# Performance work log

Hardware: AMD Instinct MI355X
Metric: run time of the kernel (lower is better)

## Reference

```python
import jax, jax.numpy as jnp
import numpy as np
from jax import lax

EPS = 1e-5

def conv2d(x, w, b=None, pad=1):
    # x: [N,C,H,W], w: [O,I,kh,kw]
    out = lax.conv_general_dilated(x, w, window_strides=(1, 1),
                                   padding=[(pad, pad), (pad, pad)],
                                   dimension_numbers=('NCHW', 'OIHW', 'NCHW'))
    if b is not None:
        out = out + b[None, :, None, None]
    return out

def batchnorm(x, gamma, beta):
    # training-mode BN (biased batch stats), matching torch default train()
    mean = jnp.mean(x, axis=(0, 2, 3), keepdims=True)
    var = jnp.var(x, axis=(0, 2, 3), keepdims=True)
    xn = (x - mean) * lax.rsqrt(var + EPS)
    return xn * gamma[None, :, None, None] + beta[None, :, None, None]

def setup_inputs() -> dict:
    key = jax.random.key(0)
    ks = jax.random.split(key, 16)
    B, Cin, H, W = 4, 3, 256, 256
    Cout = 128
    NP = 32
    npat = NP // 3  # 10 per normal region
    qc_in = Cout + 3 * npat + NP  # 190 (actual concat width)

    def kaiming(k, shape, fan_in):
        return jax.random.normal(k, shape, jnp.float32) * np.sqrt(2.0 / fan_in)

    inp = {
        'x': jax.random.normal(ks[0], (B, Cin, H, W), jnp.float32),
        'conv1_w': kaiming(ks[1], (Cout // 2, Cin, 3, 3), Cin * 9),
        'conv1_b': jnp.zeros((Cout // 2,), jnp.float32),
        'bn1_g': jnp.ones((Cout // 2,), jnp.float32),
        'bn1_b': jnp.zeros((Cout // 2,), jnp.float32),
        'conv2_w': kaiming(ks[2], (Cout, Cout // 2, 3, 3), (Cout // 2) * 9),
        'conv2_b': jnp.zeros((Cout,), jnp.float32),
        'bn2_g': jnp.ones((Cout,), jnp.float32),
        'bn2_b': jnp.zeros((Cout,), jnp.float32),
        'core_p': jax.random.normal(ks[3], (npat, Cout, 3, 3), jnp.float32),
        'clad_p': jax.random.normal(ks[4], (npat, Cout, 3, 3), jnp.float32),
        'ferr_p': jax.random.normal(ks[5], (npat, Cout, 3, 3), jnp.float32),
        'anom_p': jax.random.normal(ks[6], (NP, Cout, 3, 3), jnp.float32),
        'qa1_w': kaiming(ks[7], (64, qc_in, 1, 1), qc_in),
        'qa1_b': jnp.zeros((64,), jnp.float32),
        'qa2_w': kaiming(ks[8], (1, 64, 1, 1), 64),
        'qa2_b': jnp.zeros((1,), jnp.float32),
        'cls_w': kaiming(ks[9], (4, qc_in, 1, 1), qc_in),
        'cls_b': jnp.zeros((4,), jnp.float32),
    }
    return inp

def reference(x, conv1_w, conv1_b, bn1_g, bn1_b, conv2_w, conv2_b, bn2_g, bn2_b,
              core_p, clad_p, ferr_p, anom_p, qa1_w, qa1_b, qa2_w, qa2_b, cls_w, cls_b):
    # feature extractor: conv-bn-relu x2
    h = jax.nn.relu(batchnorm(conv2d(x, conv1_w, conv1_b), bn1_g, bn1_b))
    features = jax.nn.relu(batchnorm(conv2d(h, conv2_w, conv2_b), bn2_g, bn2_b))

    # pattern matching: the per-pattern loop of 1-out-channel convs + sigmoid
    # is exactly one multi-output-channel conv (no bias) + sigmoid
    normal_w = jnp.concatenate([core_p, clad_p, ferr_p], axis=0)  # [30,C,3,3]
    all_matches = jax.nn.sigmoid(conv2d(features, normal_w))       # [B,30,H,W]
    anomaly_matches = jax.nn.sigmoid(conv2d(features, anom_p))     # [B,32,H,W]

    quality_input = jnp.concatenate([features, all_matches, anomaly_matches], axis=1)
    q = jax.nn.relu(conv2d(quality_input, qa1_w, qa1_b, pad=0))
    quality_scores = jax.nn.sigmoid(conv2d(q, qa2_w, qa2_b, pad=0))

    classifications = conv2d(quality_input, cls_w, cls_b, pad=0)
    region_logits = classifications[:, :3]
    anomaly_logits = classifications[:, 3:4]
    region_probs = jax.nn.softmax(region_logits, axis=1)
    anomaly_probs = jax.nn.sigmoid(anomaly_logits)

    return (features, region_logits, anomaly_logits, all_matches,
            anomaly_matches, quality_scores, region_probs, anomaly_probs)
```

## Files before the change

### kernel.cpp

```cpp
#include <hip/hip_runtime.h>
#include <hip/hip_bf16.h>

typedef unsigned short u16;
typedef __attribute__((ext_vector_type(8)))  short s8v;
typedef __attribute__((ext_vector_type(4)))  short s4v;
typedef __attribute__((ext_vector_type(16))) float f16v;

#define HWX 65536
#define EPSV 1e-5f

#define O0 0u
#define O1 33554432u
#define O2 34340864u
#define O3 34603008u
#define O4 42467328u
#define O5 50855936u
#define O6 51118080u
#define O7 51904512u

__device__ __forceinline__ float u2f(u16 u) {
    union { unsigned int i; float f; } v; v.i = ((unsigned int)u) << 16; return v.f;
}
__device__ __forceinline__ u16 f2u(float f) {
    __hip_bfloat16 h = __float2bfloat16(f);
    return *reinterpret_cast<u16*>(&h);
}
__device__ __forceinline__ s8v ld8(const u16* p) {
    union { s8v v; s4v h[2]; } r;
    r.h[0] = *(const s4v*)p;
    r.h[1] = *(const s4v*)(p + 4);
    return r.v;
}

#define PHYS(i) ((i) + ((i) >> 5))

__global__ __launch_bounds__(256) void k_conv1(const float* __restrict__ x,
                                               const float* __restrict__ w,
                                               const float* __restrict__ bias,
                                               u16* __restrict__ out,
                                               float* __restrict__ ssum,
                                               float* __restrict__ sqsum) {
    const int h = blockIdx.x, cb = blockIdx.y, b = blockIdx.z;
    const int t = threadIdx.x;
    const int pg = t & 31, cg = t >> 5;
    const int px0 = pg * 8, c0 = cg * 4;
    const int cbase = cb * 32;

    __shared__ float xs[3][3][266];
    __shared__ float wl[27 * 33];

    float acc[4][8];
    #pragma unroll
    for (int c = 0; c < 4; c++) {
        float bv = bias[cbase + c0 + c];
        #pragma unroll
        for (int p = 0; p < 8; p++) acc[c][p] = bv;
    }

    for (int idx = t; idx < 3 * 768; idx += 256) {
        int ci = idx / 768, rem = idx - ci * 768;
        int r = rem >> 8, px = rem & 255;
        int hh = h + r - 1;
        float v = 0.f;
        if ((unsigned)hh < 256u)
            v = x[((size_t)(b * 3 + ci) * 256 + hh) * 256 + px];
        xs[ci][r][PHYS(1 + px)] = v;
    }
    if (t < 18) {
        int ci = t / 6, rr = t - ci * 6;
        xs[ci][rr >> 1][(rr & 1) ? PHYS(257) : 0] = 0.f;
    }
    for (int idx = t; idx < 27 * 32; idx += 256) {
        int co = idx / 27, rem = idx - co * 27;
        wl[rem * 33 + co] = w[(cbase + co) * 27 + rem];
    }
    __syncthreads();

    for (int ci = 0; ci < 3; ci++) {
        #pragma unroll
        for (int kh = 0; kh < 3; kh++) {
            float xv[10];
            #pragma unroll
            for (int j = 0; j < 10; j++) xv[j] = xs[ci][kh][PHYS(px0 + j)];
            float wv[3][4];
            #pragma unroll
            for (int kw = 0; kw < 3; kw++)
                #pragma unroll
                for (int c = 0; c < 4; c++)
                    wv[kw][c] = wl[(ci * 9 + kh * 3 + kw) * 33 + c0 + c];
            #pragma unroll
            for (int c = 0; c < 4; c++)
                #pragma unroll
                for (int p = 0; p < 8; p++)
                    acc[c][p] += xv[p] * wv[0][c] + xv[p + 1] * wv[1][c]
                               + xv[p + 2] * wv[2][c];
        }
    }

    #pragma unroll
    for (int c = 0; c < 4; c++) {
        int cm = cbase + c0 + c;
        u16* op = out + (((size_t)(b * 64 + cm) * 256 + h) * 256 + px0);
        #pragma unroll
        for (int p = 0; p < 8; p++) op[p] = f2u(acc[c][p]);
    }

    __syncthreads();
    float* red = &xs[0][0][0];
    #pragma unroll
    for (int c = 0; c < 4; c++) {
        float sv = 0.f, qv = 0.f;
        #pragma unroll
        for (int p = 0; p < 8; p++) { sv += acc[c][p]; qv += acc[c][p] * acc[c][p]; }
        red[(c0 + c) * 33 + pg] = sv;
        red[1056 + (c0 + c) * 33 + pg] = qv;
    }
    __syncthreads();
    if (t < 64) {
        int co = t & 31, v = t >> 5;
        const float* base = red + v * 1056 + co * 33;
        float sum = 0.f;
        #pragma unroll
        for (int i = 0; i < 32; i++) sum += base[i];
        atomicAdd((v ? sqsum : ssum) + cbase + co, sum);
    }
}

__global__ void k_finalize(const float* __restrict__ s, const float* __restrict__ q,
                           const float* __restrict__ g, const float* __restrict__ be,
                           float* __restrict__ sc, float* __restrict__ sh, int C) {
    int c = threadIdx.x;
    if (c >= C) return;
    const float invN = 1.f / 262144.f;
    float m = s[c] * invN;
    float v = fmaxf(q[c] * invN - m * m, 0.f);
    float scale = g[c] * rsqrtf(v + EPSV);
    sc[c] = scale;
    sh[c] = be[c] - m * scale;
}

__global__ __launch_bounds__(256) void k_bnrelu_h(ushort4* __restrict__ buf,
                                                  const float* __restrict__ sc,
                                                  const float* __restrict__ sh) {
    size_t i = (size_t)blockIdx.x * 256 + threadIdx.x;
    int c = (int)(i >> 14) & 63;
    float s = sc[c], h0 = sh[c];
    ushort4 r = buf[i];
    ushort4 o;
    o.x = f2u(fmaxf(u2f(r.x) * s + h0, 0.f));
    o.y = f2u(fmaxf(u2f(r.y) * s + h0, 0.f));
    o.z = f2u(fmaxf(u2f(r.z) * s + h0, 0.f));
    o.w = f2u(fmaxf(u2f(r.w) * s + h0, 0.f));
    buf[i] = o;
}

__global__ __launch_bounds__(256) void k_bnrelu(float4* __restrict__ buf,
                                                const float* __restrict__ sc,
                                                const float* __restrict__ sh, int C) {
    size_t i = (size_t)blockIdx.x * 256 + threadIdx.x;
    int c = (int)(i >> 14) % C;
    float s = sc[c], h0 = sh[c];
    float4 r = buf[i];
    float4 o;
    o.x = fmaxf(r.x * s + h0, 0.f);
    o.y = fmaxf(r.y * s + h0, 0.f);
    o.z = fmaxf(r.z * s + h0, 0.f);
    o.w = fmaxf(r.w * s + h0, 0.f);
    buf[i] = o;
}

__global__ __launch_bounds__(256) void k_stats(const float* __restrict__ raw,
                                               float* __restrict__ ssum,
                                               float* __restrict__ sqsum) {
    const int co = blockIdx.x, seg = blockIdx.y;
    const int t = threadIdx.x;
    __shared__ float red[8];
    float s = 0.f, q = 0.f;
    for (int b = 0; b < 4; b++) {
        const float4* p = (const float4*)(raw + ((size_t)(b * 128 + co) * HWX) + seg * 8192);
        for (int i = t; i < 2048; i += 256) {
            float4 v = p[i];
            s += v.x + v.y + v.z + v.w;
            q += v.x * v.x + v.y * v.y + v.z * v.z + v.w * v.w;
        }
    }
    #pragma unroll
    for (int off = 32; off; off >>= 1) {
        s += __shfl_down(s, off, 64);
        q += __shfl_down(q, off, 64);
    }
    int lane = t & 63, wv = t >> 6;
    if (lane == 0) { red[wv] = s; red[4 + wv] = q; }
    __syncthreads();
    if (t == 0) atomicAdd(&ssum[co], red[0] + red[1] + red[2] + red[3]);
    else if (t == 1) atomicAdd(&sqsum[co], red[4] + red[5] + red[6] + red[7]);
}

__global__ void k_prep_w(const float* __restrict__ wcat, u16* __restrict__ wtile) {
    int i = blockIdx.x * 256 + threadIdx.x;
    if (i >= 159744) return;
    int ch = i / 19968, rem = i - ch * 19968;
    int pl = rem / 9984; rem -= pl * 9984;
    int kwco = rem / 52, k = rem - kwco * 52;
    int kw = kwco >> 6, co = kwco & 63;
    u16 v = 0;
    if (k < 48 && co < 62) {
        int kh = k >> 4, ci = ch * 16 + (k & 15);
        float f = wcat[(size_t)co * 1152 + ci * 9 + kh * 3 + kw];
        u16 hv = f2u(f);
        v = pl ? f2u(f - u2f(hv)) : hv;
    }
    wtile[i] = v;
}
__global__ void k_prep_w2(const float* __restrict__ w2, u16* __restrict__ wtile2) {
    int i = blockIdx.x * 256 + threadIdx.x;
    if (i >= 79872) return;
    int ch = i / 19968, rem = i - ch * 19968;
    int kwco = rem / 52, k = rem - kwco * 52;
    int kw = kwco >> 7, co = kwco & 127;
    u16 v = 0;
    if (k < 48) {
        int kh = k >> 4, ci = ch * 16 + (k & 15);
        v = f2u(w2[((size_t)co * 64 + ci) * 9 + kh * 3 + kw]);
    }
    wtile2[i] = v;
}
__global__ void k_prep_wh(const float* __restrict__ qa1w, const float* __restrict__ clsw,
                          u16* __restrict__ whl) {
    int i = blockIdx.x * 256 + threadIdx.x;
    if (i >= 46080) return;
    int ch = i / 3840, rem = i - ch * 3840;
    int pl = rem / 1920; rem -= pl * 1920;
    int co = rem / 20, kloc = rem - co * 20;
    u16 v = 0;
    int k = ch * 16 + kloc;
    if (kloc < 16 && k < 190 && co < 68) {
        float f = (co < 64) ? qa1w[co * 190 + k] : clsw[(co - 64) * 190 + k];
        u16 hv = f2u(f);
        v = pl ? f2u(f - u2f(hv)) : hv;
    }
    whl[i] = v;
}

__device__ __forceinline__ void load_x_c2(const u16* __restrict__ hb, int b, int ch,
                                          int h, int t, unsigned xp[24]) {
    #pragma unroll
    for (int r = 0; r < 3; r++) {
        int hh = h + r - 1;
        bool vr = (unsigned)hh < 256u;
        if (vr) {
            const u16* base = hb + ((size_t)(b * 64 + ch * 16) << 16)
                            + ((size_t)hh << 8) + t;
            #pragma unroll
            for (int ci = 0; ci < 16; ci += 2) {
                unsigned a = base[(size_t)ci << 16];
                unsigned c = base[(size_t)(ci + 1) << 16];
                xp[(r * 16 + ci) >> 1] = a | (c << 16);
            }
        } else {
            #pragma unroll
            for (int ci = 0; ci < 16; ci += 2) xp[(r * 16 + ci) >> 1] = 0u;
        }
    }
}

__device__ __forceinline__ void load_split_match(const float* __restrict__ feat,
                                                 int b, int ch, int h0, int t,
                                                 unsigned xhi[32], unsigned xlo[32]) {
    #pragma unroll
    for (int r = 0; r < 4; r++) {
        int hh = h0 + r - 1;
        if ((unsigned)hh < 256u) {
            const float* base = feat + ((size_t)(b * 128 + ch * 16) << 16)
                              + ((size_t)hh << 8) + t;
            float v[16];
            #pragma unroll
            for (int ci = 0; ci < 16; ci++)
                v[ci] = base[(size_t)ci << 16];
            #pragma unroll
            for (int ci = 0; ci < 16; ci += 2) {
                u16 ha = f2u(v[ci]), hb2 = f2u(v[ci + 1]);
                unsigned la = f2u(v[ci] - u2f(ha));
                unsigned lb = f2u(v[ci + 1] - u2f(hb2));
                xhi[(r * 16 + ci) >> 1] = (unsigned)ha | ((unsigned)hb2 << 16);
                xlo[(r * 16 + ci) >> 1] = la | (lb << 16);
            }
        }
    }
}

__global__ __launch_bounds__(256, 2) void k_conv2_mf(
    const u16* __restrict__ hb, const u16* __restrict__ wtile2,
    const float* __restrict__ bias, float* __restrict__ out)
{
    const int h = blockIdx.x, b = blockIdx.y;
    const int t = threadIdx.x, l = t & 63, wv = t >> 6;
    const int kg = (l >> 5) * 8, nn = l & 31;

    __shared__ __align__(16) u16 xs[258 * 52];
    __shared__ __align__(16) u16 wl[3 * 128 * 52];

    f16v acc[2][4];
    #pragma unroll
    for (int pt = 0; pt < 2; pt++)
        #pragma unroll
        for (int s = 0; s < 4; s++)
            #pragma unroll
            for (int r = 0; r < 16; r++) acc[pt][s][r] = 0.f;

    for (int i = t; i < 258 * 52 / 4; i += 256)
        ((ushort4*)xs)[i] = ushort4{0, 0, 0, 0};
    __syncthreads();

    unsigned xp[24];
    load_x_c2(hb, b, 0, h, t, xp);

    for (int ch = 0; ch < 4; ch++) {
        {
            const int4* src = (const int4*)(wtile2 + (size_t)ch * 19968);
            for (int i = t; i < 2496; i += 256) ((int4*)wl)[i] = src[i];
        }
        #pragma unroll
        for (int r = 0; r < 3; r++) {
            if ((unsigned)(h + r - 1) < 256u) {
                #pragma unroll
                for (int g = 0; g < 4; g++) {
                    int i0 = r * 16 + g * 4;
                    uint2 hp;
                    hp.x = xp[i0 >> 1];
                    hp.y = xp[(i0 >> 1) + 1];
                    *(uint2*)&xs[(size_t)(t + 1) * 52 + i0] = hp;
                }
            }
        }
        __syncthreads();
        if (ch < 3) load_x_c2(hb, b, ch + 1, h, t, xp);
        #pragma unroll
        for (int kw = 0; kw < 3; kw++) {
            #pragma unroll
            for (int ks = 0; ks < 3; ks++) {
                int k0 = ks * 16 + kg;
                s8v af[4], bf[2];
                #pragma unroll
                for (int s = 0; s < 4; s++)
                    af[s] = ld8(&wl[(kw * 128 + s * 32 + nn) * 52 + k0]);
                #pragma unroll
                for (int pt = 0; pt < 2; pt++)
                    bf[pt] = ld8(&xs[((wv * 2 + pt) * 32 + nn + kw) * 52 + k0]);
                #pragma unroll
                for (int pt = 0; pt < 2; pt++)
                    #pragma unroll
                    for (int s = 0; s < 4; s++)
                        acc[pt][s] = __builtin_amdgcn_mfma_f32_32x32x16_bf16(
                            af[s], bf[pt], acc[pt][s], 0, 0, 0);
            }
        }
        __syncthreads();
    }

    #pragma unroll
    for (int pt = 0; pt < 2; pt++) {
        int px = (wv * 2 + pt) * 32 + nn;
        #pragma unroll
        for (int s = 0; s < 4; s++) {
            #pragma unroll
            for (int r = 0; r < 16; r++) {
                int co = s * 32 + (r & 3) + 8 * (r >> 2) + 4 * (l >> 5);
                out[(((size_t)b * 128 + co) * 256 + h) * 256 + px] = acc[pt][s][r] + bias[co];
            }
        }
    }
}

__global__ __launch_bounds__(256, 2) void k_match_mf(
    const float* __restrict__ feat, const u16* __restrict__ wtile,
    float* __restrict__ out_all, float* __restrict__ out_anom)
{
    const int h0 = blockIdx.x * 2, b = blockIdx.y;
    const int t = threadIdx.x, l = t & 63, wv = t >> 6;
    const int kg = (l >> 5) * 8, nn = l & 31;

    __shared__ __align__(16) u16 xr[4 * 258 * 20];
    __shared__ __align__(16) u16 wl[2 * 9984];

    f16v acc[2][2][2];
    #pragma unroll
    for (int o = 0; o < 2; o++)
        #pragma unroll
        for (int pt = 0; pt < 2; pt++)
            #pragma unroll
            for (int s = 0; s < 2; s++)
                #pragma unroll
                for (int r = 0; r < 16; r++) acc[o][pt][s][r] = 0.f;

    for (int i = t; i < 4 * 258 * 20 / 4; i += 256)
        ((ushort4*)xr)[i] = ushort4{0, 0, 0, 0};
    __syncthreads();

    unsigned xhi[32], xlo[32];
    load_split_match(feat, b, 0, h0, t, xhi, xlo);

    for (int ch = 0; ch < 8; ch++) {
        {
            const int4* src = (const int4*)(wtile + (size_t)ch * 2 * 9984);
            for (int i = t; i < 2496; i += 256) ((int4*)wl)[i] = src[i];
        }
        #pragma unroll
        for (int r = 0; r < 4; r++) {
            if ((unsigned)(h0 + r - 1) < 256u) {
                u16* dst = xr + r * 5160 + (t + 1) * 20;
                #pragma unroll
                for (int g = 0; g < 4; g++) {
                    uint2 hp;
                    hp.x = xhi[r * 8 + g * 2];
                    hp.y = xhi[r * 8 + g * 2 + 1];
                    *(uint2*)&dst[g * 4] = hp;
                }
            }
        }
        __syncthreads();
        #pragma unroll
        for (int kw = 0; kw < 3; kw++) {
            #pragma unroll
            for (int ks = 0; ks < 3; ks++) {
                int k0 = ks * 16 + kg;
                s8v ah0 = ld8(&wl[(kw * 64 + nn) * 52 + k0]);
                s8v ah1 = ld8(&wl[(kw * 64 + 32 + nn) * 52 + k0]);
                s8v al0 = ld8(&wl[9984 + (kw * 64 + nn) * 52 + k0]);
                s8v al1 = ld8(&wl[9984 + (kw * 64 + 32 + nn) * 52 + k0]);
                #pragma unroll
                for (int o = 0; o < 2; o++) {
                    #pragma unroll
                    for (int pt = 0; pt < 2; pt++) {
                        s8v xf = ld8(&xr[(ks + o) * 5160
                                         + ((wv * 2 + pt) * 32 + nn + kw) * 20 + kg]);
                        acc[o][pt][0] = __builtin_amdgcn_mfma_f32_32x32x16_bf16(ah0, xf, acc[o][pt][0], 0, 0, 0);
                        acc[o][pt][0] = __builtin_amdgcn_mfma_f32_32x32x16_bf16(al0, xf, acc[o][pt][0], 0, 0, 0);
                        acc[o][pt][1] = __builtin_amdgcn_mfma_f32_32x32x16_bf16(ah1, xf, acc[o][pt][1], 0, 0, 0);
                        acc[o][pt][1] = __builtin_amdgcn_mfma_f32_32x32x16_bf16(al1, xf, acc[o][pt][1], 0, 0, 0);
                    }
                }
            }
        }
        __syncthreads();
        #pragma unroll
        for (int r = 0; r < 4; r++) {
            if ((unsigned)(h0 + r - 1) < 256u) {
                u16* dst = xr + r * 5160 + (t + 1) * 20;
                #pragma unroll
                for (int g = 0; g < 4; g++) {
                    uint2 lp;
                    lp.x = xlo[r * 8 + g * 2];
                    lp.y = xlo[r * 8 + g * 2 + 1];
                    *(uint2*)&dst[g * 4] = lp;
                }
            }
        }
        __syncthreads();
        if (ch < 7) load_split_match(feat, b, ch + 1, h0, t, xhi, xlo);
        #pragma unroll
        for (int kw = 0; kw < 3; kw++) {
            #pragma unroll
            for (int ks = 0; ks < 3; ks++) {
                int k0 = ks * 16 + kg;
                s8v ah0 = ld8(&wl[(kw * 64 + nn) * 52 + k0]);
                s8v ah1 = ld8(&wl[(kw * 64 + 32 + nn) * 52 + k0]);
                #pragma unroll
                for (int o = 0; o < 2; o++) {
                    #pragma unroll
                    for (int pt = 0; pt < 2; pt++) {
                        s8v xf = ld8(&xr[(ks + o) * 5160
                                         + ((wv * 2 + pt) * 32 + nn + kw) * 20 + kg]);
                        acc[o][pt][0] = __builtin_amdgcn_mfma_f32_32x32x16_bf16(ah0, xf, acc[o][pt][0], 0, 0, 0);
                        acc[o][pt][1] = __builtin_amdgcn_mfma_f32_32x32x16_bf16(ah1, xf, acc[o][pt][1], 0, 0, 0);
                    }
                }
            }
        }
        __syncthreads();
    }

    #pragma unroll
    for (int o = 0; o < 2; o++) {
        int h = h0 + o;
        #pragma unroll
        for (int pt = 0; pt < 2; pt++) {
            int px = (wv * 2 + pt) * 32 + nn;
            #pragma unroll
            for (int s = 0; s < 2; s++) {
                #pragma unroll
                for (int r = 0; r < 16; r++) {
                    int cm = s * 32 + (r & 3) + 8 * (r >> 2) + 4 * (l >> 5);
                    float sg = 1.f / (1.f + __expf(-acc[o][pt][s][r]));
                    if (cm < 30)
                        out_all[(((size_t)b * 30 + cm) * 256 + h) * 256 + px] = sg;
                    else if (cm < 62)
                        out_anom[(((size_t)b * 32 + cm - 30) * 256 + h) * 256 + px] = sg;
                }
            }
        }
    }
}

__device__ __forceinline__ void load_x_heads(const float* __restrict__ fb,
                                             const float* __restrict__ ab,
                                             const float* __restrict__ nb,
                                             int ch, float xv[16]) {
    #pragma unroll
    for (int ci = 0; ci < 16; ci++) {
        int k = ch * 16 + ci;
        float v;
        if (k < 128)      v = fb[(size_t)k << 16];
        else if (k < 158) v = ab[(size_t)(k - 128) << 16];
        else if (k < 190) v = nb[(size_t)(k - 158) << 16];
        else              v = 0.f;
        xv[ci] = v;
    }
}

__global__ __launch_bounds__(256, 2) void k_heads_mf(
    const float* __restrict__ dout, const u16* __restrict__ whl,
    const float* __restrict__ qa1b, const float* __restrict__ qa2w,
    const float* __restrict__ qa2b, const float* __restrict__ clsb,
    float* __restrict__ out)
{
    const int h = blockIdx.x, b = blockIdx.y;
    const int t = threadIdx.x, l = t & 63, wv = t >> 6;
    const int kg = (l >> 5) * 8, nn = l & 31;

    __shared__ __align__(16) u16 xh[256 * 20];
    __shared__ __align__(16) u16 xl[256 * 20];
    __shared__ __align__(16) u16 wl2[2 * 1920];
    __shared__ float lb[69];
    __shared__ float lw2[64];

    if (t < 64) { lb[t] = qa1b[t]; lw2[t] = qa2w[t]; }
    if (t < 4) lb[64 + t] = clsb[t];
    if (t == 0) lb[68] = qa2b[0];

    f16v acc[3][2];
    #pragma unroll
    for (int s = 0; s < 3; s++)
        #pragma unroll
        for (int pt = 0; pt < 2; pt++)
            #pragma unroll
            for (int r = 0; r < 16; r++) acc[s][pt][r] = 0.f;

    const float* fb = dout + O0 + (((size_t)b * 128) << 16) + ((size_t)h << 8) + t;
    const float* ab = dout + O3 + (((size_t)b * 30) << 16) + ((size_t)h << 8) + t;
    const float* nb = dout + O4 + (((size_t)b * 32) << 16) + ((size_t)h << 8) + t;

    float xv[16];
    load_x_heads(fb, ab, nb, 0, xv);

    #pragma unroll
    for (int ch = 0; ch < 12; ch++) {
        {
            const int4* src = (const int4*)(whl + (size_t)ch * 3840);
            for (int i = t; i < 480; i += 256) ((int4*)wl2)[i] = src[i];
        }
        #pragma unroll
        for (int g = 0; g < 4; g++) {
            int i0 = g * 4;
            u16 h0 = f2u(xv[i0 + 0]), h1 = f2u(xv[i0 + 1]);
            u16 h2 = f2u(xv[i0 + 2]), h3 = f2u(xv[i0 + 3]);
            uint2 hp, lp;
            hp.x = (unsigned)h0 | ((unsigned)h1 << 16);
            hp.y = (unsigned)h2 | ((unsigned)h3 << 16);
            lp.x = (unsigned)f2u(xv[i0 + 0] - u2f(h0))
                 | ((unsigned)f2u(xv[i0 + 1] - u2f(h1)) << 16);
            lp.y = (unsigned)f2u(xv[i0 + 2] - u2f(h2))
                 | ((unsigned)f2u(xv[i0 + 3] - u2f(h3)) << 16);
            *(uint2*)&xh[t * 20 + i0] = hp;
            *(uint2*)&xl[t * 20 + i0] = lp;
        }
        __syncthreads();
        if (ch < 11) load_x_heads(fb, ab, nb, ch + 1, xv);
        s8v xfh[2], xfl[2];
        #pragma unroll
        for (int pt = 0; pt < 2; pt++) {
            int row = (wv * 2 + pt) * 32 + nn;
            xfh[pt] = ld8(&xh[row * 20 + kg]);
            xfl[pt] = ld8(&xl[row * 20 + kg]);
        }
        #pragma unroll
        for (int s = 0; s < 3; s++) {
            s8v awh = ld8(&wl2[(s * 32 + nn) * 20 + kg]);
            s8v awl = ld8(&wl2[1920 + (s * 32 + nn) * 20 + kg]);
            #pragma unroll
            for (int pt = 0; pt < 2; pt++) {
                acc[s][pt] = __builtin_amdgcn_mfma_f32_32x32x16_bf16(awh, xfh[pt], acc[s][pt], 0, 0, 0);
                acc[s][pt] = __builtin_amdgcn_mfma_f32_32x32x16_bf16(awl, xfh[pt], acc[s][pt], 0, 0, 0);
                acc[s][pt] = __builtin_amdgcn_mfma_f32_32x32x16_bf16(awh, xfl[pt], acc[s][pt], 0, 0, 0);
            }
        }
        __syncthreads();
    }

    const int hi = l >> 5;
    #pragma unroll
    for (int pt = 0; pt < 2; pt++) {
        float qa_part = 0.f;
        #pragma unroll
        for (int m = 0; m < 2; m++)
            #pragma unroll
            for (int r = 0; r < 16; r++) {
                int row = m * 32 + (r & 3) + 8 * (r >> 2) + 4 * hi;
                float v = acc[m][pt][r] + lb[row];
                qa_part += fmaxf(v, 0.f) * lw2[row];
            }
        qa_part += __shfl_xor(qa_part, 32, 64);
        if (hi == 0) {
            int px = (wv * 2 + pt) * 32 + nn;
            size_t hw = (size_t)h * 256 + px;
            float quality = 1.f / (1.f + __expf(-(qa_part + lb[68])));
            float c0 = acc[2][pt][0] + lb[64];
            float c1 = acc[2][pt][1] + lb[65];
            float c2 = acc[2][pt][2] + lb[66];
            float c3 = acc[2][pt][3] + lb[67];
            float m0 = fmaxf(c0, fmaxf(c1, c2));
            float e0 = __expf(c0 - m0), e1 = __expf(c1 - m0), e2 = __expf(c2 - m0);
            float inv = 1.f / (e0 + e1 + e2);
            out[O1 + ((size_t)b * 3 + 0) * HWX + hw] = c0;
            out[O1 + ((size_t)b * 3 + 1) * HWX + hw] = c1;
            out[O1 + ((size_t)b * 3 + 2) * HWX + hw] = c2;
            out[O2 + (size_t)b * HWX + hw] = c3;
            out[O5 + (size_t)b * HWX + hw] = quality;
            out[O6 + ((size_t)b * 3 + 0) * HWX + hw] = e0 * inv;
            out[O6 + ((size_t)b * 3 + 1) * HWX + hw] = e1 * inv;
            out[O6 + ((size_t)b * 3 + 2) * HWX + hw] = e2 * inv;
            out[O7 + (size_t)b * HWX + hw] = 1.f / (1.f + __expf(-c3));
        }
    }
}

extern "C" void kernel_launch(void* const* d_in, const int* in_sizes, int n_in,
                              void* d_out, int out_size, void* d_ws, size_t ws_size,
                              hipStream_t stream) {
    (void)in_sizes; (void)n_in; (void)out_size; (void)ws_size;
    const float* x    = (const float*)d_in[0];
    const float* w1   = (const float*)d_in[1];
    const float* b1   = (const float*)d_in[2];
    const float* g1   = (const float*)d_in[3];
    const float* be1  = (const float*)d_in[4];
    const float* w2   = (const float*)d_in[5];
    const float* b2   = (const float*)d_in[6];
    const float* g2   = (const float*)d_in[7];
    const float* be2  = (const float*)d_in[8];
    const float* core = (const float*)d_in[9];
    const float* clad = (const float*)d_in[10];
    const float* ferr = (const float*)d_in[11];
    const float* anom = (const float*)d_in[12];
    const float* qa1w = (const float*)d_in[13];
    const float* qa1b = (const float*)d_in[14];
    const float* qa2w = (const float*)d_in[15];
    const float* qa2b = (const float*)d_in[16];
    const float* clsw = (const float*)d_in[17];
    const float* clsb = (const float*)d_in[18];

    char* ws = (char*)d_ws;
    float* stats = (float*)ws;
    float* s1 = stats + 0;
    float* q1 = stats + 64;
    float* s2 = stats + 128;
    float* q2 = stats + 256;
    float* sc1 = stats + 384;
    float* sh1 = stats + 448;
    float* sc2 = stats + 512;
    float* sh2 = stats + 640;
    u16*   hraw   = (u16*)(ws + 4096);
    float* wcat   = (float*)(ws + 33558528ull);
    u16*   wtile2 = (u16*)(ws + 33844224ull);
    u16*   wtile  = (u16*)(ws + 34004224ull);
    u16*   whl    = (u16*)wcat;
    float* dout = (float*)d_out;

    hipMemsetAsync(stats, 0, 384 * sizeof(float), stream);
    hipMemcpyAsync(wcat,             core, 10 * 1152 * 4, hipMemcpyDeviceToDevice, stream);
    hipMemcpyAsync(wcat + 10 * 1152, clad, 10 * 1152 * 4, hipMemcpyDeviceToDevice, stream);
    hipMemcpyAsync(wcat + 20 * 1152, ferr, 10 * 1152 * 4, hipMemcpyDeviceToDevice, stream);
    hipMemcpyAsync(wcat + 30 * 1152, anom, 32 * 1152 * 4, hipMemcpyDeviceToDevice, stream);

    dim3 blk(256);
    k_prep_w2<<<312, blk, 0, stream>>>(w2, wtile2);
    k_prep_w<<<624, blk, 0, stream>>>(wcat, wtile);
    k_prep_wh<<<180, blk, 0, stream>>>(qa1w, clsw, whl);

    k_conv1<<<dim3(256, 2, 4), blk, 0, stream>>>(x, w1, b1, hraw, s1, q1);
    k_finalize<<<1, 128, 0, stream>>>(s1, q1, g1, be1, sc1, sh1, 64);
    k_bnrelu_h<<<16384, blk, 0, stream>>>((ushort4*)hraw, sc1, sh1);

    k_conv2_mf<<<dim3(256, 4), blk, 0, stream>>>(hraw, wtile2, b2, dout + O0);
    k_stats<<<dim3(128, 8), blk, 0, stream>>>(dout + O0, s2, q2);
    k_finalize<<<1, 128, 0, stream>>>(s2, q2, g2, be2, sc2, sh2, 128);
    k_bnrelu<<<32768, blk, 0, stream>>>((float4*)(dout + O0), sc2, sh2, 128);

    k_match_mf<<<dim3(128, 4), blk, 0, stream>>>(dout + O0, wtile, dout + O3, dout + O4);
    k_heads_mf<<<dim3(256, 4), blk, 0, stream>>>(dout, whl, qa1b, qa2w, qa2b, clsb, dout);
}
```

Measured before the change: 610.2 us.

## Fuse BN2 statistics into conv2 epilogue and finalize into bnrelu

Conv2 now reduces per-channel sum and sum of squares in its epilogue with wave shuffles, an LDS reduction and atomics. This removes the separate stats kernel, which re-read the whole 128MB feature map. The BN finalize step is folded into the bnrelu kernel, which recomputes scale and shift per thread. The heads kernel's launch bounds are also raised to target 3 blocks per SM. The conv2 epilogue takes on extra shuffle work and more atomic traffic, and the tighter register limit on the heads kernel risks spills.

```diff
diff --git a/kernel.cpp b/kernel.cpp
--- a/kernel.cpp
+++ b/kernel.cpp
@@ -155,45 +155,24 @@
 }
 
 __global__ __launch_bounds__(256) void k_bnrelu(float4* __restrict__ buf,
-                                                const float* __restrict__ sc,
-                                                const float* __restrict__ sh, int C) {
+                                                const float* __restrict__ s,
+                                                const float* __restrict__ q,
+                                                const float* __restrict__ g,
+                                                const float* __restrict__ be, int C) {
     size_t i = (size_t)blockIdx.x * 256 + threadIdx.x;
     int c = (int)(i >> 14) % C;
-    float s = sc[c], h0 = sh[c];
+    const float invN = 1.f / 262144.f;
+    float m = s[c] * invN;
+    float var = fmaxf(q[c] * invN - m * m, 0.f);
+    float sc = g[c] * rsqrtf(var + EPSV);
+    float sh = be[c] - m * sc;
     float4 r = buf[i];
     float4 o;
-    o.x = fmaxf(r.x * s + h0, 0.f);
-    o.y = fmaxf(r.y * s + h0, 0.f);
-    o.z = fmaxf(r.z * s + h0, 0.f);
-    o.w = fmaxf(r.w * s + h0, 0.f);
+    o.x = fmaxf(r.x * sc + sh, 0.f);
+    o.y = fmaxf(r.y * sc + sh, 0.f);
+    o.z = fmaxf(r.z * sc + sh, 0.f);
+    o.w = fmaxf(r.w * sc + sh, 0.f);
     buf[i] = o;
-}
-
-__global__ __launch_bounds__(256) void k_stats(const float* __restrict__ raw,
-                                               float* __restrict__ ssum,
-                                               float* __restrict__ sqsum) {
-    const int co = blockIdx.x, seg = blockIdx.y;
-    const int t = threadIdx.x;
-    __shared__ float red[8];
-    float s = 0.f, q = 0.f;
-    for (int b = 0; b < 4; b++) {
-        const float4* p = (const float4*)(raw + ((size_t)(b * 128 + co) * HWX) + seg * 8192);
-        for (int i = t; i < 2048; i += 256) {
-            float4 v = p[i];
-            s += v.x + v.y + v.z + v.w;
-            q += v.x * v.x + v.y * v.y + v.z * v.z + v.w * v.w;
-        }
-    }
-    #pragma unroll
-    for (int off = 32; off; off >>= 1) {
-        s += __shfl_down(s, off, 64);
-        q += __shfl_down(q, off, 64);
-    }
-    int lane = t & 63, wv = t >> 6;
-    if (lane == 0) { red[wv] = s; red[4 + wv] = q; }
-    __syncthreads();
-    if (t == 0) atomicAdd(&ssum[co], red[0] + red[1] + red[2] + red[3]);
-    else if (t == 1) atomicAdd(&sqsum[co], red[4] + red[5] + red[6] + red[7]);
 }
 
 __global__ void k_prep_w(const float* __restrict__ wcat, u16* __restrict__ wtile) {
@@ -291,7 +270,8 @@
 
 __global__ __launch_bounds__(256, 2) void k_conv2_mf(
     const u16* __restrict__ hb, const u16* __restrict__ wtile2,
-    const float* __restrict__ bias, float* __restrict__ out)
+    const float* __restrict__ bias, float* __restrict__ out,
+    float* __restrict__ ssum, float* __restrict__ sqsum)
 {
     const int h = blockIdx.x, b = blockIdx.y;
     const int t = threadIdx.x, l = t & 63, wv = t >> 6;
@@ -358,17 +338,49 @@
         __syncthreads();
     }
 
-    #pragma unroll
-    for (int pt = 0; pt < 2; pt++) {
-        int px = (wv * 2 + pt) * 32 + nn;
-        #pragma unroll
-        for (int s = 0; s < 4; s++) {
-            #pragma unroll
-            for (int r = 0; r < 16; r++) {
-                int co = s * 32 + (r & 3) + 8 * (r >> 2) + 4 * (l >> 5);
-                out[(((size_t)b * 128 + co) * 256 + h) * 256 + px] = acc[pt][s][r] + bias[co];
-            }
-        }
+    float* red = (float*)xs;
+    const int hi = l >> 5;
+    const int px0 = (wv * 2 + 0) * 32 + nn;
+    const int px1 = (wv * 2 + 1) * 32 + nn;
+    #pragma unroll
+    for (int s = 0; s < 4; s++) {
+        #pragma unroll
+        for (int r = 0; r < 16; r++) {
+            int co = s * 32 + (r & 3) + 8 * (r >> 2) + 4 * hi;
+            float bv = bias[co];
+            float v0 = acc[0][s][r] + bv;
+            float v1 = acc[1][s][r] + bv;
+            size_t base = (((size_t)b * 128 + co) * 256 + h) * 256;
+            out[base + px0] = v0;
+            out[base + px1] = v1;
+            float ps = v0 + v1, pq = v0 * v0 + v1 * v1;
+            #pragma unroll
+            for (int off = 16; off; off >>= 1) {
+                ps += __shfl_xor(ps, off, 64);
+                pq += __shfl_xor(pq, off, 64);
+            }
+            if (nn == 0) {
+                int slot = (wv * 2 + hi) * 64 + s * 16 + r;
+                red[slot] = ps;
+                red[512 + slot] = pq;
+            }
+        }
+    }
+    __syncthreads();
+    if (t < 128) {
+        int co = t;
+        int w32 = co & 31, si = co >> 5;
+        int hib = (w32 >> 2) & 1;
+        int ri = (w32 & 3) | (((w32 >> 3) & 3) << 2);
+        float as = 0.f, aq = 0.f;
+        #pragma unroll
+        for (int w = 0; w < 4; w++) {
+            int slot = (w * 2 + hib) * 64 + si * 16 + ri;
+            as += red[slot];
+            aq += red[512 + slot];
+        }
+        atomicAdd(&ssum[co], as);
+        atomicAdd(&sqsum[co], aq);
     }
 }
 
@@ -518,7 +530,7 @@
     }
 }
 
-__global__ __launch_bounds__(256, 2) void k_heads_mf(
+__global__ __launch_bounds__(256, 3) void k_heads_mf(
     const float* __restrict__ dout, const u16* __restrict__ whl,
     const float* __restrict__ qa1b, const float* __restrict__ qa2w,
     const float* __restrict__ qa2b, const float* __restrict__ clsb,
@@ -666,8 +678,6 @@
     float* q2 = stats + 256;
     float* sc1 = stats + 384;
     float* sh1 = stats + 448;
-    float* sc2 = stats + 512;
-    float* sh2 = stats + 640;
     u16*   hraw   = (u16*)(ws + 4096);
     float* wcat   = (float*)(ws + 33558528ull);
     u16*   wtile2 = (u16*)(ws + 33844224ull);
@@ -690,10 +700,8 @@
     k_finalize<<<1, 128, 0, stream>>>(s1, q1, g1, be1, sc1, sh1, 64);
     k_bnrelu_h<<<16384, blk, 0, stream>>>((ushort4*)hraw, sc1, sh1);
 
-    k_conv2_mf<<<dim3(256, 4), blk, 0, stream>>>(hraw, wtile2, b2, dout + O0);
-    k_stats<<<dim3(128, 8), blk, 0, stream>>>(dout + O0, s2, q2);
-    k_finalize<<<1, 128, 0, stream>>>(s2, q2, g2, be2, sc2, sh2, 128);
-    k_bnrelu<<<32768, blk, 0, stream>>>((float4*)(dout + O0), sc2, sh2, 128);
+    k_conv2_mf<<<dim3(256, 4), blk, 0, stream>>>(hraw, wtile2, b2, dout + O0, s2, q2);
+    k_bnrelu<<<32768, blk, 0, stream>>>((float4*)(dout + O0), s2, q2, g2, be2, 128);
 
     k_match_mf<<<dim3(128, 4), blk, 0, stream>>>(dout + O0, wtile, dout + O3, dout + O4);
     k_heads_mf<<<dim3(256, 4), blk, 0, stream>>>(dout, whl, qa1b, qa2w, qa2b, clsb, dout);
```

Result: slower. 736.5 us (+20.7%).
